# Optimization experiments

Hardware: AMD Instinct MI355X
Metric: run time of the kernel (lower is better)

## Reference

```python
import jax, jax.numpy as jnp
import numpy as np

N_NODES = 100000
N_EDGES = 1600000
F_IN, HIDDEN, N_CLASS = 64, 48, 40


def setup_inputs() -> dict:
    key = jax.random.key(0)
    ks = jax.random.split(key, 9)
    def glorot(k, fi, fo):
        s = (6.0 / (fi + fo)) ** 0.5
        return jax.random.uniform(k, (fi, fo), jnp.float32, -s, s)
    return {
        "x": jax.random.normal(ks[0], (N_NODES, F_IN), jnp.float32),
        "edge_index": jax.random.randint(ks[1], (2, N_EDGES), 0, N_NODES, jnp.int64),
        "edge_weight": jax.random.uniform(ks[2], (N_EDGES,), jnp.float32),
        "W1": glorot(ks[3], F_IN, HIDDEN),   # ARMAConv init_weight (K=1)
        "V1": glorot(ks[4], F_IN, HIDDEN),   # ARMAConv root_weight
        "b1": jnp.zeros((HIDDEN,), jnp.float32),
        "W2": glorot(ks[5], HIDDEN, N_CLASS),
        "V2": glorot(ks[6], HIDDEN, N_CLASS),
        "b2": jnp.zeros((N_CLASS,), jnp.float32),
    }


def _arma_conv(x, W, V, b, src, dst, norm, num_nodes):
    # out = ReLU( A_norm @ (x @ W) + x @ V + b )   (num_stacks=1, num_layers=1)
    h = x @ W                                   # [N, F_out]
    msg = h[src] * norm[:, None]                # gather + scale  [E, F_out]
    agg = jax.ops.segment_sum(msg, dst, num_segments=num_nodes)  # scatter-add
    return jax.nn.relu(agg + x @ V + b)


def reference(x, edge_index, edge_weight, W1, V1, b1, W2, V2, b2):
    num_nodes = x.shape[0]
    src, dst = edge_index[0], edge_index[1]
    # gcn_norm, add_self_loops=False: D^{-1/2} A D^{-1/2}
    deg = jax.ops.segment_sum(edge_weight, dst, num_segments=num_nodes)
    dinv = jnp.where(deg > 0, jax.lax.rsqrt(jnp.where(deg > 0, deg, 1.0)), 0.0)
    norm = dinv[src] * edge_weight * dinv[dst]
    # eval mode: input dropout is identity
    h = _arma_conv(x, W1, V1, b1, src, dst, norm, num_nodes)
    h = _arma_conv(h, W2, V2, b2, src, dst, norm, num_nodes)
    return jax.nn.log_softmax(h, axis=-1)
```

## Files before the change

kernel.cpp:

```cpp
#include <hip/hip_runtime.h>
#include <math.h>


constexpr int F_IN = 64;
constexpr int HIDDEN = 48;
constexpr int N_CLASS = 40;
constexpr int CHUNK = 4096;
constexpr int EPT = CHUNK / 256;
constexpr int BIN_SHIFT = 9;
constexpr int BIN_CAP = 9216;
constexpr int CSR_CAP = 12288;
constexpr int H1S = 56;

typedef __attribute__((ext_vector_type(8))) short bf16x8;
typedef __attribute__((ext_vector_type(4))) float f32x4;

__device__ __forceinline__ short bfr(float f) {
    unsigned u = __float_as_uint(f);
    return (short)((u + 0x7fffu + ((u >> 16) & 1u)) >> 16);
}
__device__ __forceinline__ unsigned pack_bf2(float a, float b) {
    unsigned ua = __float_as_uint(a), ub = __float_as_uint(b);
    ua = (ua + 0x7fffu + ((ua >> 16) & 1u)) >> 16;
    ub = (ub + 0x7fffu + ((ub >> 16) & 1u)) >> 16;
    return ua | (ub << 16);
}
__device__ __forceinline__ float2 unpack_bf2(unsigned u) {
    return make_float2(__uint_as_float(u << 16), __uint_as_float(u & 0xffff0000u));
}
__device__ __forceinline__ bf16x8 cvt8(float4 f0, float4 f1) {
    bf16x8 r;
    r[0] = bfr(f0.x); r[1] = bfr(f0.y); r[2] = bfr(f0.z); r[3] = bfr(f0.w);
    r[4] = bfr(f1.x); r[5] = bfr(f1.y); r[6] = bfr(f1.z); r[7] = bfr(f1.w);
    return r;
}

__global__ void init_cursor(int* __restrict__ binCursor) {
    binCursor[threadIdx.x] = (int)threadIdx.x * BIN_CAP;
}

__global__ __launch_bounds__(256) void gemm1_binscatter(
    const float* __restrict__ X, const float* __restrict__ W,
    const float* __restrict__ V, const float* __restrict__ b,
    unsigned* __restrict__ XWp, unsigned* __restrict__ AGGp, int N,
    const int* __restrict__ src, const int* __restrict__ dst,
    const float* __restrict__ w, int* __restrict__ binCursor,
    int2* __restrict__ binned, int E, int nSc) {
    __shared__ char smem[36864];
    int tid = threadIdx.x;

    if ((int)blockIdx.x < nSc) {
        int* hist = (int*)smem;
        hist[tid] = 0;
        __syncthreads();
        long long e0 = (long long)blockIdx.x * CHUNK;
        int M = (int)min((long long)CHUNK, (long long)E - e0);
        int dv[EPT], sv[EPT], wv[EPT];
#pragma unroll
        for (int q = 0; q < EPT; ++q) {
            int i = tid + q * 256;
            if (i < M) {
                dv[q] = dst[e0 + i];
                sv[q] = src[e0 + i];
                wv[q] = __float_as_int(w[e0 + i]);
                atomicAdd(&hist[dv[q] >> BIN_SHIFT], 1);
            }
        }
        __syncthreads();
        int h = hist[tid];
        int base = h ? atomicAdd(&binCursor[tid], h) : 0;
        __syncthreads();
        hist[tid] = base;
        __syncthreads();
#pragma unroll
        for (int q = 0; q < EPT; ++q) {
            int i = tid + q * 256;
            if (i < M) {
                int d = dv[q];
                int p = atomicAdd(&hist[d >> BIN_SHIFT], 1);
                binned[p] = make_int2(((d & 511) << 17) | sv[q], wv[q]);
            }
        }
        return;
    }

    short* sWT = (short*)smem;
    float* ep = (float*)(smem + 12288);
    for (int i = tid; i < 96 * 64; i += 256) {
        int c = i >> 6, k = i & 63;
        float v = (c < 48) ? W[k * 48 + c] : V[k * 48 + (c - 48)];
        sWT[i] = bfr(v);
    }
    __syncthreads();

    int lane = tid & 63, wvq = tid >> 6;
    int m = lane & 15, quad = lane >> 4;
    int nb0 = ((int)blockIdx.x - nSc) * 64;
    int n = nb0 + wvq * 16 + m;

    bf16x8 a0, a1;
    if (n < N) {
        const float4* xr = (const float4*)(X + (size_t)n * 64 + quad * 8);
        a0 = cvt8(xr[0], xr[1]);
        const float4* xr2 = (const float4*)(X + (size_t)n * 64 + 32 + quad * 8);
        a1 = cvt8(xr2[0], xr2[1]);
    } else {
        for (int j = 0; j < 8; ++j) { a0[j] = 0; a1[j] = 0; }
    }

    f32x4 acc[6];
#pragma unroll
    for (int ct = 0; ct < 6; ++ct) acc[ct] = (f32x4){0.f, 0.f, 0.f, 0.f};
#pragma unroll
    for (int ct = 0; ct < 6; ++ct) {
        bf16x8 b0 = *(const bf16x8*)(sWT + (ct * 16 + m) * 64 + quad * 8);
        bf16x8 b1 = *(const bf16x8*)(sWT + (ct * 16 + m) * 64 + 32 + quad * 8);
        acc[ct] = __builtin_amdgcn_mfma_f32_16x16x32_bf16(a0, b0, acc[ct], 0, 0, 0);
        acc[ct] = __builtin_amdgcn_mfma_f32_16x16x32_bf16(a1, b1, acc[ct], 0, 0, 0);
    }
#pragma unroll
    for (int ct = 0; ct < 6; ++ct)
#pragma unroll
        for (int r = 0; r < 4; ++r)
            ep[(wvq * 16 + quad * 4 + r) * 96 + ct * 16 + m] = acc[ct][r];
    __syncthreads();
    for (int i = tid; i < 64 * 24; i += 256) {
        int r = i / 24, c2 = i - r * 24;
        int node = nb0 + r;
        if (node >= N) continue;
        float w0 = ep[r * 96 + 2 * c2], w1 = ep[r * 96 + 2 * c2 + 1];
        XWp[node * 24 + c2] = pack_bf2(w0, w1);
        float v0 = ep[r * 96 + 48 + 2 * c2], v1 = ep[r * 96 + 48 + 2 * c2 + 1];
        float2 bb = ((const float2*)b)[c2];
        AGGp[node * 24 + c2] = pack_bf2(v0 + bb.x, v1 + bb.y);
    }
}

__global__ __launch_bounds__(512) void build_csr(const int2* __restrict__ binned,
                                                 const int* __restrict__ binCursor,
                                                 int* __restrict__ rowBeg,
                                                 int* __restrict__ rowEnd,
                                                 float* __restrict__ dinv,
                                                 unsigned* __restrict__ csr,
                                                 unsigned* __restrict__ XW1p, int N) {
    __shared__ int sx[CSR_CAP];
    __shared__ int sw[CSR_CAP];
    __shared__ int cntL[512];
    __shared__ float degL[512];
    __shared__ int scanL[512];
    int b = blockIdx.x, tid = threadIdx.x;
    int e0 = b * BIN_CAP;
    int M = min(binCursor[b] - e0, BIN_CAP);
    cntL[tid] = 0;
    degL[tid] = 0.f;
    __syncthreads();
    for (int i = tid; i < M; i += 512) {
        int2 p = binned[e0 + i];
        sx[i] = p.x;
        sw[i] = p.y;
        int dl = ((unsigned)p.x) >> 17;
        atomicAdd(&cntL[dl], 1);
        atomicAdd(&degL[dl], __int_as_float(p.y));
    }
    __syncthreads();
    int v = cntL[tid];
    scanL[tid] = v;
    __syncthreads();
#pragma unroll
    for (int o = 1; o < 512; o <<= 1) {
        int u = (tid >= o) ? scanL[tid - o] : 0;
        __syncthreads();
        scanL[tid] += u;
        __syncthreads();
    }
    int excl = scanL[tid] - v;
    int node = (b << BIN_SHIFT) + tid;
    float dg = degL[tid];
    float dv = dg > 0.f ? rsqrtf(dg) : 0.f;
    if (node < N) {
        rowBeg[node] = e0 + excl;
        rowEnd[node] = e0 + excl + v;
        dinv[node] = dv;
    }
    cntL[tid] = e0 + excl;
    degL[tid] = dv;
    __syncthreads();
    for (int i = tid; i < M; i += 512) {
        int px = sx[i], pw = sw[i];
        int dl = ((unsigned)px) >> 17;
        int pos = atomicAdd(&cntL[dl], 1);
        float wn = __int_as_float(pw) * degL[dl];
        unsigned uw = __float_as_uint(wn);
        uw = (uw + 0x7fffu + ((uw >> 16) & 1u)) >> 16;
        csr[pos] = ((unsigned)(px & 0x1FFFF) << 15) | uw;
    }
    int nb0 = b << BIN_SHIFT;
    for (int i = tid; i < 512 * 24; i += 512) {
        int nl = i / 24, c = i - nl * 24;
        int nn = nb0 + nl;
        if (nn >= N) break;
        float dvn = degL[nl];
        float2 u = unpack_bf2(XW1p[nn * 24 + c]);
        XW1p[nn * 24 + c] = pack_bf2(u.x * dvn, u.y * dvn);
    }
}

template <int W>
__device__ __forceinline__ void edge1w(const unsigned* __restrict__ XWp,
                                       unsigned p, int c, float4& s0, float4& s1) {
    uint4 u = *(const uint4*)(XWp + (p >> 15) * W + c);
    float nr = __uint_as_float((p & 0x7FFFu) << 16);
    float2 x0 = unpack_bf2(u.x), x1 = unpack_bf2(u.y);
    float2 x2 = unpack_bf2(u.z), x3 = unpack_bf2(u.w);
    s0.x = fmaf(x0.x, nr, s0.x); s0.y = fmaf(x0.y, nr, s0.y);
    s0.z = fmaf(x1.x, nr, s0.z); s0.w = fmaf(x1.y, nr, s0.w);
    s1.x = fmaf(x2.x, nr, s1.x); s1.y = fmaf(x2.y, nr, s1.y);
    s1.z = fmaf(x3.x, nr, s1.z); s1.w = fmaf(x3.y, nr, s1.w);
}

template <int W>
__device__ __forceinline__ void edge4w(const unsigned* __restrict__ XWp, uint4 p4,
                                       int c, float4& s0, float4& s1) {
    uint4 u0 = *(const uint4*)(XWp + (p4.x >> 15) * W + c);
    uint4 u1 = *(const uint4*)(XWp + (p4.y >> 15) * W + c);
    uint4 u2 = *(const uint4*)(XWp + (p4.z >> 15) * W + c);
    uint4 u3 = *(const uint4*)(XWp + (p4.w >> 15) * W + c);
    float n0 = __uint_as_float((p4.x & 0x7FFFu) << 16);
    float n1 = __uint_as_float((p4.y & 0x7FFFu) << 16);
    float n2 = __uint_as_float((p4.z & 0x7FFFu) << 16);
    float n3 = __uint_as_float((p4.w & 0x7FFFu) << 16);
    {
        float2 a0 = unpack_bf2(u0.x), a1 = unpack_bf2(u0.y);
        float2 a2 = unpack_bf2(u0.z), a3 = unpack_bf2(u0.w);
        s0.x = fmaf(a0.x, n0, s0.x); s0.y = fmaf(a0.y, n0, s0.y);
        s0.z = fmaf(a1.x, n0, s0.z); s0.w = fmaf(a1.y, n0, s0.w);
        s1.x = fmaf(a2.x, n0, s1.x); s1.y = fmaf(a2.y, n0, s1.y);
        s1.z = fmaf(a3.x, n0, s1.z); s1.w = fmaf(a3.y, n0, s1.w);
    }
    {
        float2 a0 = unpack_bf2(u1.x), a1 = unpack_bf2(u1.y);
        float2 a2 = unpack_bf2(u1.z), a3 = unpack_bf2(u1.w);
        s0.x = fmaf(a0.x, n1, s0.x); s0.y = fmaf(a0.y, n1, s0.y);
        s0.z = fmaf(a1.x, n1, s0.z); s0.w = fmaf(a1.y, n1, s0.w);
        s1.x = fmaf(a2.x, n1, s1.x); s1.y = fmaf(a2.y, n1, s1.y);
        s1.z = fmaf(a3.x, n1, s1.z); s1.w = fmaf(a3.y, n1, s1.w);
    }
    {
        float2 a0 = unpack_bf2(u2.x), a1 = unpack_bf2(u2.y);
        float2 a2 = unpack_bf2(u2.z), a3 = unpack_bf2(u2.w);
        s0.x = fmaf(a0.x, n2, s0.x); s0.y = fmaf(a0.y, n2, s0.y);
        s0.z = fmaf(a1.x, n2, s0.z); s0.w = fmaf(a1.y, n2, s0.w);
        s1.x = fmaf(a2.x, n2, s1.x); s1.y = fmaf(a2.y, n2, s1.y);
        s1.z = fmaf(a3.x, n2, s1.z); s1.w = fmaf(a3.y, n2, s1.w);
    }
    {
        float2 a0 = unpack_bf2(u3.x), a1 = unpack_bf2(u3.y);
        float2 a2 = unpack_bf2(u3.z), a3 = unpack_bf2(u3.w);
        s0.x = fmaf(a0.x, n3, s0.x); s0.y = fmaf(a0.y, n3, s0.y);
        s0.z = fmaf(a1.x, n3, s0.z); s0.w = fmaf(a1.y, n3, s0.w);
        s1.x = fmaf(a2.x, n3, s1.x); s1.y = fmaf(a2.y, n3, s1.y);
        s1.z = fmaf(a3.x, n3, s1.z); s1.w = fmaf(a3.y, n3, s1.w);
    }
}

template <int W>
__device__ __forceinline__ void row_accum4(const unsigned* __restrict__ XWp,
                                           const unsigned* __restrict__ csr,
                                           int j, int end, int c,
                                           float4& s0, float4& s1) {
    while (j < end && (j & 3)) {
        edge1w<W>(XWp, csr[j++], c, s0, s1);
    }
    int nch = (end - j) >> 2;
    if (nch > 0) {
        uint4 p4 = *(const uint4*)(csr + j);
        for (int k = 1; k < nch; ++k) {
            uint4 p4n = *(const uint4*)(csr + j + (k << 2));
            edge4w<W>(XWp, p4, c, s0, s1);
            p4 = p4n;
        }
        edge4w<W>(XWp, p4, c, s0, s1);
        j += nch << 2;
    }
    for (; j < end; ++j) {
        edge1w<W>(XWp, csr[j], c, s0, s1);
    }
}

__global__ __launch_bounds__(384) void pull_gemm2(
    const unsigned* __restrict__ XWp, const unsigned* __restrict__ csr,
    const int* __restrict__ rowBeg, const int* __restrict__ rowEnd,
    const unsigned* __restrict__ AGG1p, const float* __restrict__ W,
    const float* __restrict__ V, const float* __restrict__ b,
    const float* __restrict__ dinv, unsigned* __restrict__ XW2p,
    unsigned* __restrict__ AGG2p, int N) {
    __shared__ short sWT[80 * 64];
    __shared__ short h1s[64 * H1S];
    __shared__ float sdv[64];
    int tid = threadIdx.x;
    int nb0 = (int)blockIdx.x * 64;

    for (int i = tid; i < 80 * 64; i += 384) {
        int c = i >> 6, k = i & 63;
        float v = 0.f;
        if (k < 48) v = (c < 40) ? W[k * 40 + c] : V[k * 40 + (c - 40)];
        sWT[i] = bfr(v);
    }

    int nl = tid / 6, c1 = tid - nl * 6;
    int n = nb0 + nl;
    int c = 4 * c1;
    if (c1 == 0) sdv[nl] = (n < N) ? dinv[n] : 0.f;
    if (n < N) {
        uint4 a = *(const uint4*)(AGG1p + n * 24 + c);
        float2 f0 = unpack_bf2(a.x), f1 = unpack_bf2(a.y);
        float2 f2 = unpack_bf2(a.z), f3 = unpack_bf2(a.w);
        float4 s0 = make_float4(f0.x, f0.y, f1.x, f1.y);
        float4 s1 = make_float4(f2.x, f2.y, f3.x, f3.y);
        row_accum4<24>(XWp, csr, rowBeg[n], rowEnd[n], c, s0, s1);
        uint4 o;
        o.x = pack_bf2(fmaxf(s0.x, 0.f), fmaxf(s0.y, 0.f));
        o.y = pack_bf2(fmaxf(s0.z, 0.f), fmaxf(s0.w, 0.f));
        o.z = pack_bf2(fmaxf(s1.x, 0.f), fmaxf(s1.y, 0.f));
        o.w = pack_bf2(fmaxf(s1.z, 0.f), fmaxf(s1.w, 0.f));
        *(uint4*)(h1s + nl * H1S + 8 * c1) = o;
    } else {
        uint4 z = make_uint4(0, 0, 0, 0);
        *(uint4*)(h1s + nl * H1S + 8 * c1) = z;
    }
    __syncthreads();

    if (tid < 256) {
        int lane = tid & 63, wv = tid >> 6;
        int m = lane & 15, quad = lane >> 4;
        bf16x8 a0 = *(const bf16x8*)(h1s + (wv * 16 + m) * H1S + quad * 8);
        bf16x8 a1;
        if (quad < 2) {
            a1 = *(const bf16x8*)(h1s + (wv * 16 + m) * H1S + 32 + quad * 8);
        } else {
            for (int j = 0; j < 8; ++j) a1[j] = 0;
        }
        f32x4 acc[5];
#pragma unroll
        for (int ct = 0; ct < 5; ++ct) acc[ct] = (f32x4){0.f, 0.f, 0.f, 0.f};
#pragma unroll
        for (int ct = 0; ct < 5; ++ct) {
            bf16x8 b0 = *(const bf16x8*)(sWT + (ct * 16 + m) * 64 + quad * 8);
            bf16x8 b1 = *(const bf16x8*)(sWT + (ct * 16 + m) * 64 + 32 + quad * 8);
            acc[ct] = __builtin_amdgcn_mfma_f32_16x16x32_bf16(a0, b0, acc[ct], 0, 0, 0);
            acc[ct] = __builtin_amdgcn_mfma_f32_16x16x32_bf16(a1, b1, acc[ct], 0, 0, 0);
        }
        bool wlane = (m & 1) == 0;
#pragma unroll
        for (int ct = 0; ct < 5; ++ct) {
            int col = ct * 16 + m;
#pragma unroll
            for (int r = 0; r < 4; ++r) {
                float v = acc[ct][r];
                float vn = __shfl_xor(v, 1);
                int row = wv * 16 + quad * 4 + r;
                int node = nb0 + row;
                if (wlane && node < N) {
                    if (col < 40) {
                        float dv = sdv[row];
                        XW2p[node * 20 + (col >> 1)] = pack_bf2(v * dv, vn * dv);
                    } else {
                        float2 bb = *(const float2*)(b + (col - 40));
                        AGG2p[node * 20 + ((col - 40) >> 1)] =
                            pack_bf2(v + bb.x, vn + bb.y);
                    }
                }
            }
        }
    }
}

__global__ __launch_bounds__(320) void pull_ls(const unsigned* __restrict__ XWp,
                                               const unsigned* __restrict__ csr,
                                               const int* __restrict__ rowBeg,
                                               const int* __restrict__ rowEnd,
                                               const unsigned* __restrict__ AGG2p,
                                               float* __restrict__ out, int N) {
    __shared__ float4 sbuf[64 * 10];
    __shared__ float sl[64];
    int tid = threadIdx.x;
    int nl = tid / 5, c1 = tid - nl * 5;
    int n = blockIdx.x * 64 + nl;
    int c = 4 * c1;
    float4 s0 = make_float4(0.f, 0.f, 0.f, 0.f);
    float4 s1 = make_float4(0.f, 0.f, 0.f, 0.f);
    if (n < N) {
        uint4 a = *(const uint4*)(AGG2p + n * 20 + c);
        float2 f0 = unpack_bf2(a.x), f1 = unpack_bf2(a.y);
        float2 f2 = unpack_bf2(a.z), f3 = unpack_bf2(a.w);
        s0 = make_float4(f0.x, f0.y, f1.x, f1.y);
        s1 = make_float4(f2.x, f2.y, f3.x, f3.y);
        row_accum4<20>(XWp, csr, rowBeg[n], rowEnd[n], c, s0, s1);
    }
    sbuf[(nl * 5 + c1) * 2] = s0;
    sbuf[(nl * 5 + c1) * 2 + 1] = s1;
    __syncthreads();
    if (tid < 64) {
        float m = 0.f;
        for (int k = 0; k < 10; ++k) {
            float4 v = sbuf[tid * 10 + k];
            m = fmaxf(m, fmaxf(fmaxf(v.x, v.y), fmaxf(v.z, v.w)));
        }
        float sum = 0.f;
        for (int k = 0; k < 10; ++k) {
            float4 v = sbuf[tid * 10 + k];
            sum += expf(fmaxf(v.x, 0.f) - m) + expf(fmaxf(v.y, 0.f) - m) +
                   expf(fmaxf(v.z, 0.f) - m) + expf(fmaxf(v.w, 0.f) - m);
        }
        sl[tid] = m + logf(sum);
    }
    __syncthreads();
    if (n < N) {
        float l = sl[nl];
        float4* op = (float4*)(out + (size_t)n * 40 + 8 * c1);
        op[0] = make_float4(fmaxf(s0.x, 0.f) - l, fmaxf(s0.y, 0.f) - l,
                            fmaxf(s0.z, 0.f) - l, fmaxf(s0.w, 0.f) - l);
        op[1] = make_float4(fmaxf(s1.x, 0.f) - l, fmaxf(s1.y, 0.f) - l,
                            fmaxf(s1.z, 0.f) - l, fmaxf(s1.w, 0.f) - l);
    }
}

extern "C" void kernel_launch(void* const* d_in, const int* in_sizes, int n_in,
                              void* d_out, int out_size, void* d_ws, size_t ws_size,
                              hipStream_t stream) {
    const float* x  = (const float*)d_in[0];
    const int*   ei = (const int*)d_in[1];
    const float* ew = (const float*)d_in[2];
    const float* W1 = (const float*)d_in[3];
    const float* V1 = (const float*)d_in[4];
    const float* b1 = (const float*)d_in[5];
    const float* W2 = (const float*)d_in[6];
    const float* V2 = (const float*)d_in[7];
    const float* b2 = (const float*)d_in[8];
    float* out = (float*)d_out;

    const int N = in_sizes[0] / F_IN;
    const int E = in_sizes[2];
    const int* src = ei;
    const int* dst = ei + E;

    char* ws = (char*)d_ws;
    size_t off = 0;
    auto carve = [&](size_t bytes) {
        void* p = ws + off;
        off = (off + bytes + 255) & ~size_t(255);
        return p;
    };
    int*      binCursor = (int*)carve(256 * 4);
    int*      rowBeg    = (int*)carve((size_t)N * 4);
    int*      rowEnd    = (int*)carve((size_t)N * 4);
    float*    dinv      = (float*)carve((size_t)N * 4);
    int2*     binned    = (int2*)carve((size_t)256 * BIN_CAP * 8);
    unsigned* csr       = (unsigned*)carve((size_t)256 * BIN_CAP * 4);
    unsigned* xW1p      = (unsigned*)carve((size_t)N * 24 * 4);
    unsigned* agg1p     = (unsigned*)carve((size_t)N * 24 * 4);
    unsigned* xW2p      = (unsigned*)carve((size_t)N * 20 * 4);
    unsigned* agg2p     = (unsigned*)carve((size_t)N * 20 * 4);

    const int B = 256;
    auto cdiv = [](long long a, long long b) { return (int)((a + b - 1) / b); };
    const int nSc = cdiv(E, CHUNK);
    const int nBins = (N + (1 << BIN_SHIFT) - 1) >> BIN_SHIFT;
    const int nGemmBlocks = cdiv(N, 64);

    init_cursor<<<1, 256, 0, stream>>>(binCursor);
    gemm1_binscatter<<<nSc + nGemmBlocks, B, 0, stream>>>(
        x, W1, V1, b1, xW1p, agg1p, N, src, dst, ew, binCursor, binned, E, nSc);
    build_csr<<<nBins, 512, 0, stream>>>(binned, binCursor, rowBeg, rowEnd,
                                         dinv, csr, xW1p, N);

    pull_gemm2<<<nGemmBlocks, 384, 0, stream>>>(xW1p, csr, rowBeg, rowEnd,
                                                agg1p, W2, V2, b2, dinv,
                                                xW2p, agg2p, N);

    pull_ls<<<cdiv(N, 64), 320, 0, stream>>>(xW2p, csr, rowBeg, rowEnd,
                                             agg2p, out, N);
}
```

Before: 254.6 us.

## Halve CSR bin size to double build_csr blocks and drop LDS staging

Bins now cover 256 destination nodes instead of 512, which gives about 391 build_csr blocks of 256 threads instead of about 196 blocks of 512 threads. build_csr no longer stages the binned edges in large LDS arrays and instead re-reads them from global memory in the second pass, so occupancy is no longer capped by LDS. The bin cursor becomes a per-bin count with fixed offsets. In exchange the binned array is read twice, and the scatter kernel loops over more histogram entries.

```diff
diff --git a/kernel.cpp b/kernel.cpp
--- a/kernel.cpp
+++ b/kernel.cpp
@@ -7,9 +7,9 @@
 constexpr int N_CLASS = 40;
 constexpr int CHUNK = 4096;
 constexpr int EPT = CHUNK / 256;
-constexpr int BIN_SHIFT = 9;
-constexpr int BIN_CAP = 9216;
-constexpr int CSR_CAP = 12288;
+constexpr int BIN_SHIFT = 8;
+constexpr int BIN_CAP = 4608;
+constexpr int MAXBINS = 512;
 constexpr int H1S = 56;
 
 typedef __attribute__((ext_vector_type(8))) short bf16x8;
@@ -35,8 +35,8 @@
     return r;
 }
 
-__global__ void init_cursor(int* __restrict__ binCursor) {
-    binCursor[threadIdx.x] = (int)threadIdx.x * BIN_CAP;
+__global__ void init_cursor(int* __restrict__ binCursor, int NB) {
+    if ((int)threadIdx.x < NB) binCursor[threadIdx.x] = 0;
 }
 
 __global__ __launch_bounds__(256) void gemm1_binscatter(
@@ -45,13 +45,13 @@
     unsigned* __restrict__ XWp, unsigned* __restrict__ AGGp, int N,
     const int* __restrict__ src, const int* __restrict__ dst,
     const float* __restrict__ w, int* __restrict__ binCursor,
-    int2* __restrict__ binned, int E, int nSc) {
+    int2* __restrict__ binned, int E, int nSc, int NB) {
     __shared__ char smem[36864];
     int tid = threadIdx.x;
 
     if ((int)blockIdx.x < nSc) {
         int* hist = (int*)smem;
-        hist[tid] = 0;
+        for (int j = tid; j < NB; j += 256) hist[j] = 0;
         __syncthreads();
         long long e0 = (long long)blockIdx.x * CHUNK;
         int M = (int)min((long long)CHUNK, (long long)E - e0);
@@ -67,18 +67,20 @@
             }
         }
         __syncthreads();
-        int h = hist[tid];
-        int base = h ? atomicAdd(&binCursor[tid], h) : 0;
-        __syncthreads();
-        hist[tid] = base;
+        for (int j = tid; j < NB; j += 256) {
+            int h = hist[j];
+            hist[j] = h ? atomicAdd(&binCursor[j], h) : 0;
+        }
         __syncthreads();
 #pragma unroll
         for (int q = 0; q < EPT; ++q) {
             int i = tid + q * 256;
             if (i < M) {
                 int d = dv[q];
-                int p = atomicAdd(&hist[d >> BIN_SHIFT], 1);
-                binned[p] = make_int2(((d & 511) << 17) | sv[q], wv[q]);
+                int bin = d >> BIN_SHIFT;
+                int p = atomicAdd(&hist[bin], 1);
+                binned[(size_t)bin * BIN_CAP + p] =
+                    make_int2(((d & 255) << 17) | sv[q], wv[q]);
             }
         }
         return;
@@ -136,28 +138,24 @@
     }
 }
 
-__global__ __launch_bounds__(512) void build_csr(const int2* __restrict__ binned,
+__global__ __launch_bounds__(256) void build_csr(const int2* __restrict__ binned,
                                                  const int* __restrict__ binCursor,
                                                  int* __restrict__ rowBeg,
                                                  int* __restrict__ rowEnd,
                                                  float* __restrict__ dinv,
                                                  unsigned* __restrict__ csr,
                                                  unsigned* __restrict__ XW1p, int N) {
-    __shared__ int sx[CSR_CAP];
-    __shared__ int sw[CSR_CAP];
-    __shared__ int cntL[512];
-    __shared__ float degL[512];
-    __shared__ int scanL[512];
+    __shared__ int cntL[256];
+    __shared__ float degL[256];
+    __shared__ int scanL[256];
     int b = blockIdx.x, tid = threadIdx.x;
-    int e0 = b * BIN_CAP;
-    int M = min(binCursor[b] - e0, BIN_CAP);
+    size_t e0 = (size_t)b * BIN_CAP;
+    int M = min(binCursor[b], BIN_CAP);
     cntL[tid] = 0;
     degL[tid] = 0.f;
     __syncthreads();
-    for (int i = tid; i < M; i += 512) {
+    for (int i = tid; i < M; i += 256) {
         int2 p = binned[e0 + i];
-        sx[i] = p.x;
-        sw[i] = p.y;
         int dl = ((unsigned)p.x) >> 17;
         atomicAdd(&cntL[dl], 1);
         atomicAdd(&degL[dl], __int_as_float(p.y));
@@ -167,7 +165,7 @@
     scanL[tid] = v;
     __syncthreads();
 #pragma unroll
-    for (int o = 1; o < 512; o <<= 1) {
+    for (int o = 1; o < 256; o <<= 1) {
         int u = (tid >= o) ? scanL[tid - o] : 0;
         __syncthreads();
         scanL[tid] += u;
@@ -178,24 +176,24 @@
     float dg = degL[tid];
     float dv = dg > 0.f ? rsqrtf(dg) : 0.f;
     if (node < N) {
-        rowBeg[node] = e0 + excl;
-        rowEnd[node] = e0 + excl + v;
+        rowBeg[node] = (int)e0 + excl;
+        rowEnd[node] = (int)e0 + excl + v;
         dinv[node] = dv;
     }
-    cntL[tid] = e0 + excl;
+    cntL[tid] = (int)e0 + excl;
     degL[tid] = dv;
     __syncthreads();
-    for (int i = tid; i < M; i += 512) {
-        int px = sx[i], pw = sw[i];
-        int dl = ((unsigned)px) >> 17;
+    for (int i = tid; i < M; i += 256) {
+        int2 p = binned[e0 + i];
+        int dl = ((unsigned)p.x) >> 17;
         int pos = atomicAdd(&cntL[dl], 1);
-        float wn = __int_as_float(pw) * degL[dl];
+        float wn = __int_as_float(p.y) * degL[dl];
         unsigned uw = __float_as_uint(wn);
         uw = (uw + 0x7fffu + ((uw >> 16) & 1u)) >> 16;
-        csr[pos] = ((unsigned)(px & 0x1FFFF) << 15) | uw;
+        csr[pos] = ((unsigned)(p.x & 0x1FFFF) << 15) | uw;
     }
     int nb0 = b << BIN_SHIFT;
-    for (int i = tid; i < 512 * 24; i += 512) {
+    for (int i = tid; i < 256 * 24; i += 256) {
         int nl = i / 24, c = i - nl * 24;
         int nn = nb0 + nl;
         if (nn >= N) break;
@@ -444,6 +442,9 @@
     const int* src = ei;
     const int* dst = ei + E;
 
+    auto cdiv = [](long long a, long long b) { return (int)((a + b - 1) / b); };
+    const int nBins = cdiv(N, 1 << BIN_SHIFT);
+
     char* ws = (char*)d_ws;
     size_t off = 0;
     auto carve = [&](size_t bytes) {
@@ -451,27 +452,26 @@
         off = (off + bytes + 255) & ~size_t(255);
         return p;
     };
-    int*      binCursor = (int*)carve(256 * 4);
+    int*      binCursor = (int*)carve(MAXBINS * 4);
     int*      rowBeg    = (int*)carve((size_t)N * 4);
     int*      rowEnd    = (int*)carve((size_t)N * 4);
     float*    dinv      = (float*)carve((size_t)N * 4);
-    int2*     binned    = (int2*)carve((size_t)256 * BIN_CAP * 8);
-    unsigned* csr       = (unsigned*)carve((size_t)256 * BIN_CAP * 4);
+    int2*     binned    = (int2*)carve((size_t)nBins * BIN_CAP * 8);
+    unsigned* csr       = (unsigned*)carve((size_t)nBins * BIN_CAP * 4);
     unsigned* xW1p      = (unsigned*)carve((size_t)N * 24 * 4);
     unsigned* agg1p     = (unsigned*)carve((size_t)N * 24 * 4);
     unsigned* xW2p      = (unsigned*)carve((size_t)N * 20 * 4);
     unsigned* agg2p     = (unsigned*)carve((size_t)N * 20 * 4);
 
     const int B = 256;
-    auto cdiv = [](long long a, long long b) { return (int)((a + b - 1) / b); };
     const int nSc = cdiv(E, CHUNK);
-    const int nBins = (N + (1 << BIN_SHIFT) - 1) >> BIN_SHIFT;
     const int nGemmBlocks = cdiv(N, 64);
 
-    init_cursor<<<1, 256, 0, stream>>>(binCursor);
+    init_cursor<<<1, MAXBINS, 0, stream>>>(binCursor, nBins);
     gemm1_binscatter<<<nSc + nGemmBlocks, B, 0, stream>>>(
-        x, W1, V1, b1, xW1p, agg1p, N, src, dst, ew, binCursor, binned, E, nSc);
-    build_csr<<<nBins, 512, 0, stream>>>(binned, binCursor, rowBeg, rowEnd,
+        x, W1, V1, b1, xW1p, agg1p, N, src, dst, ew, binCursor, binned, E, nSc,
+        nBins);
+    build_csr<<<nBins, 256, 0, stream>>>(binned, binCursor, rowBeg, rowEnd,
                                          dinv, csr, xW1p, N);
 
     pull_gemm2<<<nGemmBlocks, 384, 0, stream>>>(xW1p, csr, rowBeg, rowEnd,
```

After: 254.7 us. No clear change (+0.0%).
